# Optimization experiments

Hardware: AMD Instinct MI355X
Metric: run time of the kernel (lower is better)

Reference implementation:

```python
import jax, jax.numpy as jnp
import numpy as np

N = 100000
IN_DIM = 512
HIDDEN = 512


def setup_inputs() -> dict:
    key = jax.random.key(0)
    ks = jax.random.split(key, 6)
    x = jax.random.normal(ks[0], (N, IN_DIM), dtype=jnp.float32)
    # neighbor-index format: up to 3 neighbors per node, -1 = padding
    edge_index = jax.random.randint(ks[1], (N, 3), -1, N, dtype=jnp.int64)
    s1 = 1.0 / np.sqrt(IN_DIM)
    s2 = 1.0 / np.sqrt(HIDDEN)
    W1 = jax.random.normal(ks[2], (HIDDEN, IN_DIM), dtype=jnp.float32) * s1
    b1 = jax.random.normal(ks[3], (HIDDEN,), dtype=jnp.float32) * s1
    W2 = jax.random.normal(ks[4], (HIDDEN, HIDDEN), dtype=jnp.float32) * s2
    b2 = jax.random.normal(ks[5], (HIDDEN,), dtype=jnp.float32) * s2
    return {"x": x, "edge_index": edge_index, "W1": W1, "b1": b1, "W2": W2, "b2": b2}


def _gcn_layer(x, edge_index, W, b):
    # degree: number of valid neighbors + 1 (self), clamped to >= 1
    deg = jnp.sum(edge_index >= 0, axis=-1, keepdims=True).astype(x.dtype) + 1.0  # [N,1]
    deg = jnp.maximum(deg, 1.0)
    h = (x @ W.T + b) / jnp.sqrt(deg)  # [N,D]
    # pad with a zero row; index -1 selects the pad row (matches torch semantics)
    padded = jnp.concatenate([h, jnp.zeros((1, h.shape[1]), h.dtype)], axis=0)  # [N+1,D]
    neigh = padded[edge_index]  # [N,3,D] gather
    return (jnp.sum(neigh, axis=1) + h) / jnp.sqrt(deg)


def reference(x, edge_index, W1, b1, W2, b2):
    h = jax.nn.elu(_gcn_layer(x, edge_index, W1, b1))
    h = jax.nn.elu(_gcn_layer(h, edge_index, W2, b2))
    return h
```

## Files before the change

### kernel.cpp

```cpp
#include <hip/hip_runtime.h>
#include <cstdint>
#include <cstddef>

#define DIM 512
#define BM 128
#define BN 128
#define BK 32

typedef unsigned short ushort_t;
typedef __attribute__((ext_vector_type(8))) short short8;
typedef __attribute__((ext_vector_type(4))) float floatx4;
typedef __attribute__((address_space(3))) void lds_void;
typedef __attribute__((address_space(1))) void gbl_void;

__device__ __forceinline__ float bf2f(ushort_t s) {
    unsigned u = ((unsigned)s) << 16;
    float f;
    __builtin_memcpy(&f, &u, 4);
    return f;
}
__device__ __forceinline__ ushort_t f2bf(float f) {
    unsigned u;
    __builtin_memcpy(&u, &f, 4);
    u = u + 0x7FFFu + ((u >> 16) & 1u);
    return (ushort_t)(u >> 16);
}
__device__ __forceinline__ float elu_f(float x) { return x > 0.0f ? x : __expf(x) - 1.0f; }

__global__ void probe_kernel(const void* __restrict__ x, const void* __restrict__ e,
                             int* __restrict__ flags) {
    if (threadIdx.x != 0 || blockIdx.x != 0) return;
    const ushort_t* u = (const ushort_t*)x;
    int crazy = 0;
    for (int j = 0; j < 512; ++j) {
        const ushort_t s = u[2 * j];
        const int ex = (s >> 7) & 0xFF;
        const bool nonzero = (s & 0x7FFF) != 0;
        if (ex >= 160 || (ex < 96 && nonzero)) crazy++;
    }
    const int* w = (const int*)e;
    int se = 0;
    for (int j = 0; j < 64; ++j) {
        const int v = w[2 * j + 1];
        if (v == 0 || v == -1) se++;
    }
    flags[0] = (crazy > 64) ? 1 : 0;
    flags[1] = (se >= 60) ? 1 : 0;
}

__global__ void tof32_kernel(const void* __restrict__ src, float* __restrict__ dst,
                             int n, const int* __restrict__ flags) {
    const int i = blockIdx.x * blockDim.x + threadIdx.x;
    if (i < n) dst[i] = flags[0] ? ((const float*)src)[i] : bf2f(((const ushort_t*)src)[i]);
}

__global__ __launch_bounds__(256)
void split_kernel(const void* __restrict__ src, ushort_t* __restrict__ hi,
                  ushort_t* __restrict__ lo, long long n, const int* __restrict__ flags) {
    const long long i = ((long long)blockIdx.x * blockDim.x + threadIdx.x) * 8;
    if (i >= n) return;
    const bool isf32 = flags[0] != 0;
    float v[8];
    if (isf32) {
        const float* s = (const float*)src + i;
        const float4 f0 = *(const float4*)s;
        const float4 f1 = *(const float4*)(s + 4);
        v[0] = f0.x; v[1] = f0.y; v[2] = f0.z; v[3] = f0.w;
        v[4] = f1.x; v[5] = f1.y; v[6] = f1.z; v[7] = f1.w;
    } else {
        const ushort_t* s = (const ushort_t*)src + i;
        const ushort4 u0 = *(const ushort4*)s;
        const ushort4 u1 = *(const ushort4*)(s + 4);
        v[0] = bf2f(u0.x); v[1] = bf2f(u0.y); v[2] = bf2f(u0.z); v[3] = bf2f(u0.w);
        v[4] = bf2f(u1.x); v[5] = bf2f(u1.y); v[6] = bf2f(u1.z); v[7] = bf2f(u1.w);
    }
    ushort_t h[8];
    #pragma unroll
    for (int j = 0; j < 8; ++j) h[j] = f2bf(v[j]);
    ushort4 a, b;
    a.x = h[0]; a.y = h[1]; a.z = h[2]; a.w = h[3];
    b.x = h[4]; b.y = h[5]; b.z = h[6]; b.w = h[7];
    *(ushort4*)(hi + i) = a;
    *(ushort4*)(hi + i + 4) = b;
    if (lo) {
        ushort4 la, lb;
        la.x = isf32 ? f2bf(v[0] - bf2f(h[0])) : 0;
        la.y = isf32 ? f2bf(v[1] - bf2f(h[1])) : 0;
        la.z = isf32 ? f2bf(v[2] - bf2f(h[2])) : 0;
        la.w = isf32 ? f2bf(v[3] - bf2f(h[3])) : 0;
        lb.x = isf32 ? f2bf(v[4] - bf2f(h[4])) : 0;
        lb.y = isf32 ? f2bf(v[5] - bf2f(h[5])) : 0;
        lb.z = isf32 ? f2bf(v[6] - bf2f(h[6])) : 0;
        lb.w = isf32 ? f2bf(v[7] - bf2f(h[7])) : 0;
        *(ushort4*)(lo + i) = la;
        *(ushort4*)(lo + i + 4) = lb;
    }
}

__global__ void degree_kernel(const int* __restrict__ E, float* __restrict__ rdeg,
                              int n, const int* __restrict__ flags) {
    const int i = blockIdx.x * blockDim.x + threadIdx.x;
    if (i >= n) return;
    int e0, e1, e2;
    if (flags[1]) { e0 = E[i * 6 + 0]; e1 = E[i * 6 + 2]; e2 = E[i * 6 + 4]; }
    else          { e0 = E[i * 3 + 0]; e1 = E[i * 3 + 1]; e2 = E[i * 3 + 2]; }
    const int dg = 1 + (e0 >= 0) + (e1 >= 0) + (e2 >= 0);
    rdeg[i] = 1.0f / sqrtf((float)dg);
}

template <bool ALO, bool WLO, typename HT>
__global__ __launch_bounds__(256)
void gemm_gcn(const ushort_t* __restrict__ Ahi, const ushort_t* __restrict__ Alo,
              const ushort_t* __restrict__ Whi, const ushort_t* __restrict__ Wlo,
              const float* __restrict__ bias, const float* __restrict__ rdeg,
              HT* __restrict__ H, int M)
{
    constexpr int NTA = ALO ? 2 : 1;
    constexpr int NTW = WLO ? 2 : 1;
    __shared__ __align__(16) ushort_t As[NTA][BK / 8][BM][8];
    __shared__ __align__(16) ushort_t Ws[NTW][BK / 8][BN][8];

    const int tid  = threadIdx.x;
    const int wave = tid >> 6;
    const int lane = tid & 63;
    const int n_blk = blockIdx.x * BN;
    const int m_blk = blockIdx.y * BM;
    const int m_off = (wave & 1) * 64;
    const int n_off = (wave >> 1) * 64;

    floatx4 acc[4][4] = {};

    for (int k0 = 0; k0 < DIM; k0 += BK) {
        constexpr int CPW = 2 * (NTA + NTW);
        #pragma unroll
        for (int i = 0; i < CPW; ++i) {
            const int cc   = wave + i * 4;
            const int tile = cc >> 3;
            const int c    = cc & 7;
            const int kb   = c >> 1;
            const int rh   = (c & 1) * 64;
            if (tile < NTA) {
                int r = m_blk + rh + lane;
                r = r < M ? r : M - 1;
                const ushort_t* src = (tile == 0 ? Ahi : Alo) + (size_t)r * DIM + k0 + kb * 8;
                __builtin_amdgcn_global_load_lds((gbl_void*)src, (lds_void*)&As[tile][kb][rh][0], 16, 0, 0);
            } else {
                const int t = tile - NTA;
                const int r = n_blk + rh + lane;
                const ushort_t* src = (t == 0 ? Whi : Wlo) + (size_t)r * DIM + k0 + kb * 8;
                __builtin_amdgcn_global_load_lds((gbl_void*)src, (lds_void*)&Ws[t][kb][rh][0], 16, 0, 0);
            }
        }
        __syncthreads();

        const int kbb = lane >> 4;
        short8 ah[4], al[4], wh[4], wl[4];
        #pragma unroll
        for (int mi = 0; mi < 4; ++mi) {
            ah[mi] = *(const short8*)&As[0][kbb][m_off + mi * 16 + (lane & 15)][0];
            if constexpr (ALO) al[mi] = *(const short8*)&As[NTA - 1][kbb][m_off + mi * 16 + (lane & 15)][0];
        }
        #pragma unroll
        for (int ni = 0; ni < 4; ++ni) {
            wh[ni] = *(const short8*)&Ws[0][kbb][n_off + ni * 16 + (lane & 15)][0];
            if constexpr (WLO) wl[ni] = *(const short8*)&Ws[NTW - 1][kbb][n_off + ni * 16 + (lane & 15)][0];
        }
        #pragma unroll
        for (int mi = 0; mi < 4; ++mi) {
            #pragma unroll
            for (int ni = 0; ni < 4; ++ni) {
                acc[mi][ni] = __builtin_amdgcn_mfma_f32_16x16x32_bf16(ah[mi], wh[ni], acc[mi][ni], 0, 0, 0);
                if constexpr (WLO)
                    acc[mi][ni] = __builtin_amdgcn_mfma_f32_16x16x32_bf16(ah[mi], wl[ni], acc[mi][ni], 0, 0, 0);
                if constexpr (ALO)
                    acc[mi][ni] = __builtin_amdgcn_mfma_f32_16x16x32_bf16(al[mi], wh[ni], acc[mi][ni], 0, 0, 0);
            }
        }
        __syncthreads();
    }

    const int rbase = m_blk + m_off + ((lane >> 4) << 2);
    const int cbase = n_blk + n_off + (lane & 15);
    #pragma unroll
    for (int mi = 0; mi < 4; ++mi) {
        #pragma unroll
        for (int r = 0; r < 4; ++r) {
            const int row = rbase + mi * 16 + r;
            if (row < M) {
                const float rd = rdeg[row];
                #pragma unroll
                for (int ni = 0; ni < 4; ++ni) {
                    const int col = cbase + ni * 16;
                    const float v = (acc[mi][ni][r] + bias[col]) * rd;
                    if constexpr (sizeof(HT) == 4) H[(size_t)row * DIM + col] = v;
                    else *(ushort_t*)&H[(size_t)row * DIM + col] = f2bf(v);
                }
            }
        }
    }
}

template <typename HT>
__device__ __forceinline__ void addRow(const HT* H, int row, int d,
                                       float& a0, float& a1, float& a2, float& a3) {
    if constexpr (sizeof(HT) == 4) {
        const float4 v = *reinterpret_cast<const float4*>((const float*)H + (size_t)row * DIM + d);
        a0 += v.x; a1 += v.y; a2 += v.z; a3 += v.w;
    } else {
        const ushort4 v = *reinterpret_cast<const ushort4*>((const ushort_t*)H + (size_t)row * DIM + d);
        a0 += bf2f(v.x); a1 += bf2f(v.y); a2 += bf2f(v.z); a3 += bf2f(v.w);
    }
}

template <typename HT, int MODE>
__global__ __launch_bounds__(256)
void aggregate_gcn(const HT* __restrict__ H, const int* __restrict__ E,
                   const float* __restrict__ rdeg, const int* __restrict__ flags,
                   void* __restrict__ outA, ushort_t* __restrict__ outB, int n)
{
    const int node = blockIdx.x * 2 + (threadIdx.x >> 7);
    if (node >= n) return;
    const int t = threadIdx.x & 127;
    const int d = t << 2;
    int e0, e1, e2;
    if (flags[1]) { e0 = E[node * 6 + 0]; e1 = E[node * 6 + 2]; e2 = E[node * 6 + 4]; }
    else          { e0 = E[node * 3 + 0]; e1 = E[node * 3 + 1]; e2 = E[node * 3 + 2]; }
    const float rd = rdeg[node];

    float a0 = 0.f, a1 = 0.f, a2 = 0.f, a3 = 0.f;
    addRow(H, node, d, a0, a1, a2, a3);
    if (e0 >= 0) addRow(H, e0, d, a0, a1, a2, a3);
    if (e1 >= 0) addRow(H, e1, d, a0, a1, a2, a3);
    if (e2 >= 0) addRow(H, e2, d, a0, a1, a2, a3);

    a0 = elu_f(a0 * rd); a1 = elu_f(a1 * rd); a2 = elu_f(a2 * rd); a3 = elu_f(a3 * rd);

    const size_t base = (size_t)node * DIM + d;
    if constexpr (MODE == 0) {
        ushort4 h;
        h.x = f2bf(a0); h.y = f2bf(a1); h.z = f2bf(a2); h.w = f2bf(a3);
        *(ushort4*)((ushort_t*)outA + base) = h;
        if (outB) {
            ushort4 l;
            l.x = f2bf(a0 - bf2f(h.x)); l.y = f2bf(a1 - bf2f(h.y));
            l.z = f2bf(a2 - bf2f(h.z)); l.w = f2bf(a3 - bf2f(h.w));
            *(ushort4*)(outB + base) = l;
        }
    } else {
        if (flags[0]) {
            float4 o; o.x = a0; o.y = a1; o.z = a2; o.w = a3;
            *(float4*)((float*)outA + base) = o;
        } else {
            ushort4 o;
            o.x = f2bf(a0); o.y = f2bf(a1); o.z = f2bf(a2); o.w = f2bf(a3);
            *(ushort4*)((ushort_t*)outA + base) = o;
        }
    }
}

extern "C" void kernel_launch(void* const* d_in, const int* in_sizes, int n_in,
                              void* d_out, int out_size, void* d_ws, size_t ws_size,
                              hipStream_t stream) {
    const void* X  = d_in[0];
    const void* E  = d_in[1];
    const void* W1 = d_in[2];
    const void* b1 = d_in[3];
    const void* W2 = d_in[4];
    const void* b2 = d_in[5];
    const int* E32 = (const int*)E;

    const int M = in_sizes[0] / DIM;
    const long long NX = (long long)M * DIM;
    const long long NW = (long long)DIM * DIM;

    char* ws = (char*)d_ws;
    size_t off = 0;
    auto take = [&](size_t sz) { size_t o = off; off = (off + sz + 511) & ~(size_t)511; return o; };

    int*      flags = (int*)(ws + take(64));
    float*    rdeg  = (float*)(ws + take((size_t)M * 4));
    float*    b1f   = (float*)(ws + take(DIM * 4));
    float*    b2f   = (float*)(ws + take(DIM * 4));
    ushort_t* W1h   = (ushort_t*)(ws + take((size_t)NW * 2));
    ushort_t* W1l   = (ushort_t*)(ws + take((size_t)NW * 2));
    ushort_t* W2h   = (ushort_t*)(ws + take((size_t)NW * 2));
    ushort_t* W2l   = (ushort_t*)(ws + take((size_t)NW * 2));
    const size_t header = off;
    const size_t SX  = (size_t)NX * 2;
    const size_t SH4 = (size_t)NX * 4;
    const size_t SH2 = (size_t)NX * 2;

    int tier;
    if      (ws_size >= header + 2 * SX + SH4 + 1024) tier = 0;
    else if (ws_size >= header + SX + SH4 + 1024)     tier = 1;
    else                                              tier = 2;

    ushort_t* Xh = (ushort_t*)(ws + take(SX));
    ushort_t* Xl = (tier == 0) ? (ushort_t*)(ws + take(SX)) : nullptr;
    void*     H  = ws + take(tier <= 1 ? SH4 : SH2);

    probe_kernel<<<1, 1, 0, stream>>>(X, E, flags);
    tof32_kernel<<<2, 256, 0, stream>>>(b1, b1f, DIM, flags);
    tof32_kernel<<<2, 256, 0, stream>>>(b2, b2f, DIM, flags);

    const int gW = (int)((NW / 8 + 255) / 256);
    const int gX = (int)((NX / 8 + 255) / 256);
    split_kernel<<<gW, 256, 0, stream>>>(W1, W1h, tier <= 1 ? W1l : nullptr, NW, flags);
    split_kernel<<<gW, 256, 0, stream>>>(W2, W2h, tier <= 1 ? W2l : nullptr, NW, flags);
    split_kernel<<<gX, 256, 0, stream>>>(X, Xh, Xl, NX, flags);
    degree_kernel<<<(M + 255) / 256, 256, 0, stream>>>(E32, rdeg, M, flags);

    const dim3 gG(DIM / BN, (M + BM - 1) / BM);
    const dim3 gA((M + 1) / 2);

    if (tier == 0) {
        gemm_gcn<true, true, float><<<gG, 256, 0, stream>>>(Xh, Xl, W1h, W1l, b1f, rdeg, (float*)H, M);
        aggregate_gcn<float, 0><<<gA, 256, 0, stream>>>((const float*)H, E32, rdeg, flags, Xh, Xl, M);
        gemm_gcn<true, true, float><<<gG, 256, 0, stream>>>(Xh, Xl, W2h, W2l, b2f, rdeg, (float*)H, M);
        aggregate_gcn<float, 1><<<gA, 256, 0, stream>>>((const float*)H, E32, rdeg, flags, d_out, nullptr, M);
    } else if (tier == 1) {
        gemm_gcn<false, true, float><<<gG, 256, 0, stream>>>(Xh, nullptr, W1h, W1l, b1f, rdeg, (float*)H, M);
        aggregate_gcn<float, 0><<<gA, 256, 0, stream>>>((const float*)H, E32, rdeg, flags, Xh, nullptr, M);
        gemm_gcn<false, true, float><<<gG, 256, 0, stream>>>(Xh, nullptr, W2h, W2l, b2f, rdeg, (float*)H, M);
        aggregate_gcn<float, 1><<<gA, 256, 0, stream>>>((const float*)H, E32, rdeg, flags, d_out, nullptr, M);
    } else {
        gemm_gcn<false, false, ushort_t><<<gG, 256, 0, stream>>>(Xh, nullptr, W1h, nullptr, b1f, rdeg, (ushort_t*)H, M);
        aggregate_gcn<ushort_t, 0><<<gA, 256, 0, stream>>>((const ushort_t*)H, E32, rdeg, flags, Xh, nullptr, M);
        gemm_gcn<false, false, ushort_t><<<gG, 256, 0, stream>>>(Xh, nullptr, W2h, nullptr, b2f, rdeg, (ushort_t*)H, M);
        aggregate_gcn<ushort_t, 1><<<gA, 256, 0, stream>>>((const ushort_t*)H, E32, rdeg, flags, d_out, nullptr, M);
    }
}
```

Before: 1.274 ms.

## Double-buffer LDS tiles in GEMM and swizzle workgroups across XCDs

Converts the GEMM main loop to double-buffered LDS staging: the next K tile is loaded via global_load_lds while the current tile is computed, with explicit vmcnt waits and raw barriers replacing the two __syncthreads. It also remaps block IDs so consecutive tiles land on the same XCD for better L2 reuse of A/W rows. This aims to hide global load latency and improve cache locality, at the cost of twice the LDS footprint (possibly lower occupancy) and hand-tuned wait counts that must match the number of issued loads.

Result: faster. 1.245 ms (-2.3%).

```diff
diff --git a/kernel.cpp b/kernel.cpp
--- a/kernel.cpp
+++ b/kernel.cpp
@@ -117,21 +117,31 @@
 {
     constexpr int NTA = ALO ? 2 : 1;
     constexpr int NTW = WLO ? 2 : 1;
-    __shared__ __align__(16) ushort_t As[NTA][BK / 8][BM][8];
-    __shared__ __align__(16) ushort_t Ws[NTW][BK / 8][BN][8];
+    constexpr int CPW = 2 * (NTA + NTW);
+    constexpr int NXB = DIM / BN;
+    constexpr int NT  = DIM / BK;
+    __shared__ __align__(16) ushort_t As[2][NTA][BK / 8][BM][8];
+    __shared__ __align__(16) ushort_t Ws[2][NTW][BK / 8][BN][8];
 
     const int tid  = threadIdx.x;
     const int wave = tid >> 6;
     const int lane = tid & 63;
-    const int n_blk = blockIdx.x * BN;
-    const int m_blk = blockIdx.y * BM;
+
+    const int nwg = NXB * gridDim.y;
+    const int bid = blockIdx.y * NXB + blockIdx.x;
+    const int q = nwg >> 3, rm = nwg & 7;
+    const int xcd = bid & 7, lin = bid >> 3;
+    const int swz = (xcd < rm ? xcd * (q + 1) : rm * (q + 1) + (xcd - rm) * q) + lin;
+    const int n_blk = (swz & (NXB - 1)) * BN;
+    const int m_blk = (swz / NXB) * BM;
+
     const int m_off = (wave & 1) * 64;
     const int n_off = (wave >> 1) * 64;
 
     floatx4 acc[4][4] = {};
 
-    for (int k0 = 0; k0 < DIM; k0 += BK) {
-        constexpr int CPW = 2 * (NTA + NTW);
+    auto stage = [&](int buf, int t) {
+        const int k0 = t * BK;
         #pragma unroll
         for (int i = 0; i < CPW; ++i) {
             const int cc   = wave + i * 4;
@@ -143,27 +153,28 @@
                 int r = m_blk + rh + lane;
                 r = r < M ? r : M - 1;
                 const ushort_t* src = (tile == 0 ? Ahi : Alo) + (size_t)r * DIM + k0 + kb * 8;
-                __builtin_amdgcn_global_load_lds((gbl_void*)src, (lds_void*)&As[tile][kb][rh][0], 16, 0, 0);
+                __builtin_amdgcn_global_load_lds((gbl_void*)src, (lds_void*)&As[buf][tile][kb][rh][0], 16, 0, 0);
             } else {
-                const int t = tile - NTA;
+                const int tt = tile - NTA;
                 const int r = n_blk + rh + lane;
-                const ushort_t* src = (t == 0 ? Whi : Wlo) + (size_t)r * DIM + k0 + kb * 8;
-                __builtin_amdgcn_global_load_lds((gbl_void*)src, (lds_void*)&Ws[t][kb][rh][0], 16, 0, 0);
+                const ushort_t* src = (tt == 0 ? Whi : Wlo) + (size_t)r * DIM + k0 + kb * 8;
+                __builtin_amdgcn_global_load_lds((gbl_void*)src, (lds_void*)&Ws[buf][tt][kb][rh][0], 16, 0, 0);
             }
         }
-        __syncthreads();
-
+    };
+
+    auto compute = [&](int buf) {
         const int kbb = lane >> 4;
         short8 ah[4], al[4], wh[4], wl[4];
         #pragma unroll
         for (int mi = 0; mi < 4; ++mi) {
-            ah[mi] = *(const short8*)&As[0][kbb][m_off + mi * 16 + (lane & 15)][0];
-            if constexpr (ALO) al[mi] = *(const short8*)&As[NTA - 1][kbb][m_off + mi * 16 + (lane & 15)][0];
+            ah[mi] = *(const short8*)&As[buf][0][kbb][m_off + mi * 16 + (lane & 15)][0];
+            if constexpr (ALO) al[mi] = *(const short8*)&As[buf][NTA - 1][kbb][m_off + mi * 16 + (lane & 15)][0];
         }
         #pragma unroll
         for (int ni = 0; ni < 4; ++ni) {
-            wh[ni] = *(const short8*)&Ws[0][kbb][n_off + ni * 16 + (lane & 15)][0];
-            if constexpr (WLO) wl[ni] = *(const short8*)&Ws[NTW - 1][kbb][n_off + ni * 16 + (lane & 15)][0];
+            wh[ni] = *(const short8*)&Ws[buf][0][kbb][n_off + ni * 16 + (lane & 15)][0];
+            if constexpr (WLO) wl[ni] = *(const short8*)&Ws[buf][NTW - 1][kbb][n_off + ni * 16 + (lane & 15)][0];
         }
         #pragma unroll
         for (int mi = 0; mi < 4; ++mi) {
@@ -176,8 +187,23 @@
                     acc[mi][ni] = __builtin_amdgcn_mfma_f32_16x16x32_bf16(al[mi], wh[ni], acc[mi][ni], 0, 0, 0);
             }
         }
-        __syncthreads();
-    }
+    };
+
+    stage(0, 0);
+    #pragma unroll 2
+    for (int t = 0; t < NT - 1; ++t) {
+        const int cur = t & 1;
+        stage(cur ^ 1, t + 1);
+        if constexpr (CPW == 8)      asm volatile("s_waitcnt vmcnt(8)" ::: "memory");
+        else if constexpr (CPW == 6) asm volatile("s_waitcnt vmcnt(6)" ::: "memory");
+        else                         asm volatile("s_waitcnt vmcnt(4)" ::: "memory");
+        __builtin_amdgcn_s_barrier();
+        compute(cur);
+        __builtin_amdgcn_s_barrier();
+    }
+    asm volatile("s_waitcnt vmcnt(0)" ::: "memory");
+    __builtin_amdgcn_s_barrier();
+    compute((NT - 1) & 1);
 
     const int rbase = m_blk + m_off + ((lane >> 4) << 2);
     const int cbase = n_blk + n_off + (lane & 15);
```
